# Optimization experiments

Measured on AMD Instinct MI355X. Metric: run time of the kernel, lower is better.

Reference implementation:

```python
import jax, jax.numpy as jnp
import numpy as np

B, CIN, COUT, K, SDIM, H, W = 16, 512, 512, 3, 512, 64, 64


def setup_inputs() -> dict:
    key = jax.random.key(0)
    k1, k2, k3, k4 = jax.random.split(key, 4)
    return {
        "x": jax.random.normal(k1, (B, CIN, H, W), dtype=jnp.float32),
        "style": jax.random.normal(k2, (B, SDIM), dtype=jnp.float32),
        "weight": jax.random.normal(k3, (COUT, CIN, K, K), dtype=jnp.float32),
        "style_w": jax.random.normal(k4, (CIN, SDIM), dtype=jnp.float32),
        "style_b": jnp.ones((CIN,), dtype=jnp.float32),  # bias.data.fill_(1.0)
    }


def reference(x, style, weight, style_w, style_b):
    batch, in_ch, h, w_size = x.shape
    out_ch, _, ks, _ = weight.shape
    pad = ks // 2
    # EqualizedLinear: runtime weight scaling by 1/sqrt(fan_in)
    lin_scale = 1.0 / np.sqrt(style_w.shape[1])
    s = style @ (style_w * lin_scale).T + style_b  # [B, Cin]
    # modulate
    conv_scale = 1.0 / np.sqrt(in_ch * ks * ks)
    wmod = (weight[None] * conv_scale) * s[:, None, :, None, None]  # [B,Cout,Cin,k,k]
    # demodulate
    dcoef = jax.lax.rsqrt(jnp.sum(jnp.square(wmod), axis=(2, 3, 4)) + 1e-8)  # [B,Cout]
    wmod = wmod * dcoef[:, :, None, None, None]
    # grouped conv with groups = batch
    x_r = x.reshape(1, batch * in_ch, h, w_size)
    w_r = wmod.reshape(batch * out_ch, in_ch, ks, ks)
    out = jax.lax.conv_general_dilated(
        x_r, w_r,
        window_strides=(1, 1),
        padding=[(pad, pad), (pad, pad)],
        dimension_numbers=("NCHW", "OIHW", "NCHW"),
        feature_group_count=batch,
    )
    return out.reshape(batch, out_ch, h, w_size)
```

## Files before the change

### kernel.cpp

```cpp
#include <hip/hip_runtime.h>
#include <math.h>

#define B 16
#define CIN 512
#define COUT 512
#define SDIM 512
#define H 64
#define W 64

typedef short s16x8 __attribute__((ext_vector_type(8)));
typedef float f32x4 __attribute__((ext_vector_type(4)));
typedef float f32x16 __attribute__((ext_vector_type(16)));

__device__ __constant__ float LIN_SCALE  = 0.04419417382415922f;
__device__ __constant__ float CONV_SCALE = 0.014731391274719742f;

__device__ __forceinline__ ushort f2bf(float f) {
  unsigned u = __float_as_uint(f);
  return (ushort)((u + 0x7FFFu + ((u >> 16) & 1u)) >> 16);
}

__device__ __forceinline__ int slot_swz(int col, int o) {
  return ((col & 1) * 4 + o) ^ ((col >> 1) & 7);
}

#define GLOAD16(g, l)                                           \
  __builtin_amdgcn_global_load_lds(                             \
      (const __attribute__((address_space(1))) unsigned*)(g),   \
      (__attribute__((address_space(3))) unsigned*)(l), 16, 0, 0)

__global__ __launch_bounds__(512) void style_mod_kernel(
    const float* __restrict__ style, const float* __restrict__ style_w,
    const float* __restrict__ style_b, float* __restrict__ s,
    float* __restrict__ s2) {
  const int b = blockIdx.x;
  const int ci = threadIdx.x;
  __shared__ float st[SDIM];
  st[ci] = style[b * SDIM + ci];
  __syncthreads();

  const float4* wr = reinterpret_cast<const float4*>(style_w + (size_t)ci * SDIM);
  float acc = 0.f;
#pragma unroll 4
  for (int k = 0; k < SDIM / 4; ++k) {
    float4 wv = wr[k];
    acc += st[4 * k + 0] * wv.x + st[4 * k + 1] * wv.y +
           st[4 * k + 2] * wv.z + st[4 * k + 3] * wv.w;
  }
  float v = acc * LIN_SCALE + style_b[ci];
  s[b * CIN + ci] = v;
  s2[b * CIN + ci] = v * v;
}

__global__ __launch_bounds__(512) void dcoef_kernel(
    const float* __restrict__ s2, const float* __restrict__ wsq,
    float* __restrict__ outscale) {
  const int b = blockIdx.x;
  const int co = threadIdx.x;
  __shared__ float sh[CIN];
  sh[co] = s2[b * CIN + co];
  __syncthreads();

  const float4* wr = reinterpret_cast<const float4*>(wsq + (size_t)co * CIN);
  float acc = 0.f;
#pragma unroll 4
  for (int k = 0; k < CIN / 4; ++k) {
    float4 wv = wr[k];
    acc += sh[4 * k + 0] * wv.x + sh[4 * k + 1] * wv.y +
           sh[4 * k + 2] * wv.z + sh[4 * k + 3] * wv.w;
  }
  float d = rsqrtf(acc * CONV_SCALE * CONV_SCALE + 1e-8f);
  outscale[b * COUT + co] = d * CONV_SCALE;
}

__global__ __launch_bounds__(256) void pack_w_kernel(
    const float* __restrict__ w, ushort* __restrict__ wt,
    float* __restrict__ wsq) {
  const int t = blockIdx.x * 256 + threadIdx.x;
  const int s = t & 3;
  const int chunk = (t >> 2) & 15;
  const int co = t >> 6;
  const float4* wp =
      (const float4*)(w + ((size_t)co * 512 + chunk * 32 + s * 8) * 9);
  float wv[72];
#pragma unroll
  for (int i = 0; i < 18; ++i) {
    float4 v = wp[i];
    wv[4 * i + 0] = v.x; wv[4 * i + 1] = v.y;
    wv[4 * i + 2] = v.z; wv[4 * i + 3] = v.w;
  }
  {
    float q[8];
#pragma unroll
    for (int i = 0; i < 8; ++i) {
      float a = 0.f;
#pragma unroll
      for (int k = 0; k < 9; ++k) {
        float v = wv[i * 9 + k];
        a += v * v;
      }
      q[i] = a;
    }
    float4* qd = (float4*)(wsq + (size_t)co * 512 + chunk * 32 + s * 8);
    qd[0] = make_float4(q[0], q[1], q[2], q[3]);
    qd[1] = make_float4(q[4], q[5], q[6], q[7]);
  }
  const int sp = slot_swz(co, s);
  ushort* dst = wt + (size_t)chunk * 147456 + (size_t)(co >> 1) * 64 + sp * 8;
#pragma unroll
  for (int j = 0; j < 9; ++j) {
    s16x8 p;
#pragma unroll
    for (int i = 0; i < 8; ++i) p[i] = (short)f2bf(wv[i * 9 + j]);
    *(s16x8*)(dst + (size_t)j * 16384) = p;
  }
}

__global__ __launch_bounds__(256) void pack_x_kernel(
    const float* __restrict__ x, const float* __restrict__ smod,
    ushort* __restrict__ xp) {
  __shared__ float xt[32][65];
  __shared__ float sm[32];
  const int tid = threadIdx.x;
  const int gr = blockIdx.x, chunk = blockIdx.y, b = blockIdx.z;
  if (tid < 32) sm[tid] = smod[b * 512 + chunk * 32 + tid];
  {
    const int ci = tid >> 3, cq = tid & 7;
    const float4* rp = (const float4*)(
        x + (((size_t)b * 512 + chunk * 32 + ci) * 64 + gr) * 64 + cq * 8);
    float4 a = rp[0], c2 = rp[1];
    float* row = &xt[ci][cq * 8];
    row[0] = a.x; row[1] = a.y; row[2] = a.z; row[3] = a.w;
    row[4] = c2.x; row[5] = c2.y; row[6] = c2.z; row[7] = c2.w;
  }
  __syncthreads();
  const int c = tid >> 2, o = tid & 3;
  s16x8 p;
#pragma unroll
  for (int i = 0; i < 8; ++i)
    p[i] = (short)f2bf(xt[o * 8 + i][c] * sm[o * 8 + i]);
  const int cc = c + 1;
  const int off_us = (cc >> 1) * 64 + slot_swz(cc, o) * 8 - 32;
  *(s16x8*)(xp + ((size_t)(b * 16 + chunk) * 64 + gr) * 2048 + off_us) = p;
}

#define XS4OFF 36864
#define DLDS4 79104

__global__ __launch_bounds__(256, 2) void conv_mfma6_kernel(
    const ushort* __restrict__ wt, const ushort* __restrict__ xp,
    const float* __restrict__ outscale, float* __restrict__ out) {
  extern __shared__ char smem[];

  const int tid = threadIdx.x;
  const int hb = blockIdx.x;
  const int cb = blockIdx.y;
  const int b  = blockIdx.z;
  const int h0 = hb * 8, co0 = cb * 64;
  const int lane = tid & 63, wid = tid >> 6;
  const int l31 = lane & 31, hi = lane >> 5;

  {
    s16x8* p = (s16x8*)(smem + XS4OFF);
    for (int e = tid; e < 2640; e += 256) p[e] = (s16x8)0;
  }

  f32x16 acc[2][2][2];
#pragma unroll
  for (int rr = 0; rr < 2; ++rr)
#pragma unroll
    for (int mt = 0; mt < 2; ++mt)
#pragma unroll
      for (int nt = 0; nt < 2; ++nt) acc[rr][mt][nt] = (f32x16)0.f;

  int aoff[2][2];
#pragma unroll
  for (int mt = 0; mt < 2; ++mt)
#pragma unroll
    for (int ks = 0; ks < 2; ++ks) {
      int co = mt * 32 + l31;
      aoff[mt][ks] = (co >> 1) * 128 + slot_swz(co, ks * 2 + hi) * 16;
    }
  int boff[3][2][2];
#pragma unroll
  for (int kw = 0; kw < 3; ++kw)
#pragma unroll
    for (int nt = 0; nt < 2; ++nt)
#pragma unroll
      for (int ks = 0; ks < 2; ++ks) {
        int cc = nt * 32 + l31 + kw;
        boff[kw][nt][ks] = (cc >> 1) * 128 + slot_swz(cc, ks * 2 + hi) * 16;
      }

  const char* wsrc0 = (const char*)wt + cb * 4096 + tid * 16;
  const char* xsrc0 = (const char*)xp + (size_t)b * 4194304 + tid * 16;
  char* wdst = smem + tid * 16;
  char* xdst = smem + XS4OFF + 64 + tid * 16;
  const char* wb = smem;
  const char* xb = smem + XS4OFF + 2 * wid * 4224;

  __syncthreads();

  for (int chunk = 0; chunk < 16; ++chunk) {
    const char* wsrc = wsrc0 + (size_t)chunk * 294912;
    const char* xsrc = xsrc0 + (size_t)chunk * 262144;
#pragma unroll
    for (int t = 0; t < 9; ++t)
      GLOAD16(wsrc + t * 32768, wdst + t * 4096);
#pragma unroll
    for (int t = 0; t < 10; ++t) {
      int gr = h0 - 1 + t;
      if ((unsigned)gr < 64u)
        GLOAD16(xsrc + (size_t)gr * 4096, xdst + t * 4224);
    }
    __syncthreads();

#pragma unroll
    for (int kw = 0; kw < 3; ++kw) {
      s16x8 bf[4][2][2];
#pragma unroll
      for (int q = 0; q < 4; ++q)
#pragma unroll
        for (int nt = 0; nt < 2; ++nt)
#pragma unroll
          for (int ks = 0; ks < 2; ++ks)
            bf[q][nt][ks] =
                *(const s16x8*)(xb + q * 4224 + boff[kw][nt][ks]);
#pragma unroll
      for (int kh = 0; kh < 3; ++kh) {
        const char* wj = wb + (kh * 3 + kw) * 4096;
#pragma unroll
        for (int ks = 0; ks < 2; ++ks) {
          s16x8 af0 = *(const s16x8*)(wj + aoff[0][ks]);
          s16x8 af1 = *(const s16x8*)(wj + aoff[1][ks]);
#pragma unroll
          for (int rr = 0; rr < 2; ++rr)
#pragma unroll
            for (int nt = 0; nt < 2; ++nt) {
              acc[rr][0][nt] = __builtin_amdgcn_mfma_f32_32x32x16_bf16(
                  af0, bf[rr + kh][nt][ks], acc[rr][0][nt], 0, 0, 0);
              acc[rr][1][nt] = __builtin_amdgcn_mfma_f32_32x32x16_bf16(
                  af1, bf[rr + kh][nt][ks], acc[rr][1][nt], 0, 0, 0);
            }
        }
      }
    }
    __syncthreads();
  }

#pragma unroll
  for (int mt = 0; mt < 2; ++mt) {
#pragma unroll
    for (int reg = 0; reg < 16; ++reg) {
      const int row = (reg & 3) + 8 * (reg >> 2) + 4 * hi;
      const int co = co0 + mt * 32 + row;
      const float osc = outscale[b * COUT + co];
      float* obase = out + ((size_t)b * COUT + co) * H * W;
#pragma unroll
      for (int rr = 0; rr < 2; ++rr) {
        const int h = h0 + 2 * wid + rr;
#pragma unroll
        for (int nt = 0; nt < 2; ++nt)
          obase[h * W + nt * 32 + l31] = acc[rr][mt][nt][reg] * osc;
      }
    }
  }
}

__global__ __launch_bounds__(256, 2) void conv_mfma_kernel(
    const float* __restrict__ x, const float* __restrict__ weight,
    const float* __restrict__ s, const float* __restrict__ outscale,
    float* __restrict__ out) {
  __shared__ ushort xs[6][66][32];
  __shared__ ushort ws[9][64][32];

  const int tid = threadIdx.x;
  const int hb = blockIdx.x;
  const int cb = blockIdx.y;
  const int b  = blockIdx.z;
  const int h0 = hb * 4;
  const int co0 = cb * 64;
  const int lane = tid & 63;
  const int wid = tid >> 6;
  const int l15 = lane & 15;
  const int l4  = lane >> 4;

  f32x4 acc[4][4];
#pragma unroll
  for (int mt = 0; mt < 4; ++mt)
#pragma unroll
    for (int nt = 0; nt < 4; ++nt) acc[mt][nt] = (f32x4)0.f;

  const int wq = tid & 3;
  const int wco = tid >> 2;

  for (int c0 = 0; c0 < CIN; c0 += 32) {
    {
      const float4* wp = reinterpret_cast<const float4*>(
          weight + ((size_t)(co0 + wco) * CIN + c0 + wq * 8) * 9);
      float wv[72];
#pragma unroll
      for (int t = 0; t < 18; ++t) {
        float4 v = wp[t];
        wv[4 * t + 0] = v.x; wv[4 * t + 1] = v.y;
        wv[4 * t + 2] = v.z; wv[4 * t + 3] = v.w;
      }
      float sv[8];
#pragma unroll
      for (int i = 0; i < 8; ++i) sv[i] = s[b * CIN + c0 + wq * 8 + i];
#pragma unroll
      for (int j = 0; j < 9; ++j) {
        s16x8 p;
#pragma unroll
        for (int i = 0; i < 8; ++i)
          p[i] = (short)f2bf(wv[i * 9 + j] * sv[i]);
        *reinterpret_cast<s16x8*>(&ws[j][wco][wq * 8]) = p;
      }
    }
#pragma unroll
    for (int it = 0; it < 7; ++it) {
      int e = tid + it * 256;
      if (e < 6 * 66 * 4) {
        int q = e & 3;
        int t2 = e >> 2;
        int cc = t2 % 66;
        int r = t2 / 66;
        int gr = h0 - 1 + r;
        int gc = cc - 1;
        s16x8 p;
        if ((unsigned)gr < H && (unsigned)gc < W) {
          const float* xp2 =
              x + (((size_t)b * CIN + c0 + q * 8) * H + gr) * W + gc;
#pragma unroll
          for (int i = 0; i < 8; ++i) p[i] = (short)f2bf(xp2[(size_t)i * H * W]);
        } else {
#pragma unroll
          for (int i = 0; i < 8; ++i) p[i] = 0;
        }
        *reinterpret_cast<s16x8*>(&xs[r][cc][q * 8]) = p;
      }
    }
    __syncthreads();

#pragma unroll
    for (int kh = 0; kh < 3; ++kh) {
#pragma unroll
      for (int kw = 0; kw < 3; ++kw) {
        const int j = kh * 3 + kw;
        s16x8 af[4], bf[4];
#pragma unroll
        for (int mt = 0; mt < 4; ++mt)
          af[mt] = *reinterpret_cast<const s16x8*>(
              &ws[j][mt * 16 + l15][l4 * 8]);
#pragma unroll
        for (int nt = 0; nt < 4; ++nt)
          bf[nt] = *reinterpret_cast<const s16x8*>(
              &xs[wid + kh][nt * 16 + l15 + kw][l4 * 8]);
#pragma unroll
        for (int mt = 0; mt < 4; ++mt)
#pragma unroll
          for (int nt = 0; nt < 4; ++nt)
            acc[mt][nt] = __builtin_amdgcn_mfma_f32_16x16x32_bf16(
                af[mt], bf[nt], acc[mt][nt], 0, 0, 0);
      }
    }
    __syncthreads();
  }

  const int h = h0 + wid;
#pragma unroll
  for (int mt = 0; mt < 4; ++mt) {
#pragma unroll
    for (int r = 0; r < 4; ++r) {
      const int co = co0 + mt * 16 + l4 * 4 + r;
      const float osc = outscale[b * COUT + co];
      float* orow = out + (((size_t)b * COUT + co) * H + h) * W;
#pragma unroll
      for (int nt = 0; nt < 4; ++nt)
        orow[nt * 16 + l15] = acc[mt][nt][r] * osc;
    }
  }
}

extern "C" void kernel_launch(void* const* d_in, const int* in_sizes, int n_in,
                              void* d_out, int out_size, void* d_ws,
                              size_t ws_size, hipStream_t stream) {
  const float* x = (const float*)d_in[0];
  const float* style = (const float*)d_in[1];
  const float* weight = (const float*)d_in[2];
  const float* style_w = (const float*)d_in[3];
  const float* style_b = (const float*)d_in[4];
  float* out = (float*)d_out;

  char* wsb = (char*)d_ws;
  float* s = (float*)(wsb + 0);
  float* s2 = (float*)(wsb + 32768);
  float* wsq = (float*)(wsb + 65536);
  float* outscale = (float*)(wsb + 1114112);
  ushort* wt = (ushort*)(wsb + 1146880);
  ushort* xp = (ushort*)(wsb + 5865472);
  const size_t NEED = 72974336;

  hipError_t attr_ok = hipFuncSetAttribute(
      reinterpret_cast<const void*>(conv_mfma6_kernel),
      hipFuncAttributeMaxDynamicSharedMemorySize, DLDS4);

  style_mod_kernel<<<B, 512, 0, stream>>>(style, style_w, style_b, s, s2);
  pack_w_kernel<<<128, 256, 0, stream>>>(weight, wt, wsq);
  dcoef_kernel<<<B, 512, 0, stream>>>(s2, wsq, outscale);

  if (attr_ok == hipSuccess && ws_size >= NEED) {
    pack_x_kernel<<<dim3(64, 16, 16), 256, 0, stream>>>(x, s, xp);
    conv_mfma6_kernel<<<dim3(8, 8, 16), 256, DLDS4, stream>>>(wt, xp, outscale,
                                                              out);
  } else {
    conv_mfma_kernel<<<dim3(16, 8, 16), 256, 0, stream>>>(x, weight, s,
                                                          outscale, out);
  }
}
```

Measured before the change: 345.4 us.

## Load weight MFMA fragments directly from global into registers with prefetch

Weights are repacked into per-lane MFMA fragment order so each wave reads A operands straight from global memory into registers, triple-buffered two taps ahead. This removes the weight tile from LDS, which shrinks shared memory and drops the LDS staging and reads for weights. The grid axes are also swapped so blocks sharing an input row run close together, improving reuse of the input in L2. In exchange, every wave fetches the weights itself from global or L2 memory, and the extra fragment registers raise register pressure.

```diff
diff --git a/kernel.cpp b/kernel.cpp
--- a/kernel.cpp
+++ b/kernel.cpp
@@ -105,14 +105,14 @@
     qd[0] = make_float4(q[0], q[1], q[2], q[3]);
     qd[1] = make_float4(q[4], q[5], q[6], q[7]);
   }
-  const int sp = slot_swz(co, s);
-  ushort* dst = wt + (size_t)chunk * 147456 + (size_t)(co >> 1) * 64 + sp * 8;
 #pragma unroll
   for (int j = 0; j < 9; ++j) {
     s16x8 p;
 #pragma unroll
     for (int i = 0; i < 8; ++i) p[i] = (short)f2bf(wv[i * 9 + j]);
-    *(s16x8*)(dst + (size_t)j * 16384) = p;
+    size_t frag = ((size_t)(chunk * 9 + j) * 16 + (co >> 5)) * 2 + (s >> 1);
+    size_t off = frag * 512 + (size_t)((s & 1) * 32 + (co & 31)) * 8;
+    *(s16x8*)(wt + off) = p;
   }
 }
 
@@ -144,24 +144,31 @@
   *(s16x8*)(xp + ((size_t)(b * 16 + chunk) * 64 + gr) * 2048 + off_us) = p;
 }
 
-#define XS4OFF 36864
-#define DLDS4 79104
-
-__global__ __launch_bounds__(256, 2) void conv_mfma6_kernel(
+#define DLDS7 42240
+
+#define LOADA(CK, T, BUF) {                                          \
+    const int j_ = ((T) % 3) * 3 + ((T) / 3);                        \
+    const size_t f0_ = ((size_t)((CK) * 9 + j_) * 16 + cb * 2) * 2;  \
+    af[BUF][0][0] = wfr[(f0_ + 0) * 64 + lane];                      \
+    af[BUF][0][1] = wfr[(f0_ + 1) * 64 + lane];                      \
+    af[BUF][1][0] = wfr[(f0_ + 2) * 64 + lane];                      \
+    af[BUF][1][1] = wfr[(f0_ + 3) * 64 + lane]; }
+
+__global__ __launch_bounds__(256, 2) void conv_mfma7_kernel(
     const ushort* __restrict__ wt, const ushort* __restrict__ xp,
     const float* __restrict__ outscale, float* __restrict__ out) {
   extern __shared__ char smem[];
 
   const int tid = threadIdx.x;
-  const int hb = blockIdx.x;
-  const int cb = blockIdx.y;
+  const int cb = blockIdx.x;
+  const int hb = blockIdx.y;
   const int b  = blockIdx.z;
   const int h0 = hb * 8, co0 = cb * 64;
   const int lane = tid & 63, wid = tid >> 6;
   const int l31 = lane & 31, hi = lane >> 5;
 
   {
-    s16x8* p = (s16x8*)(smem + XS4OFF);
+    s16x8* p = (s16x8*)smem;
     for (int e = tid; e < 2640; e += 256) p[e] = (s16x8)0;
   }
 
@@ -173,14 +180,6 @@
 #pragma unroll
       for (int nt = 0; nt < 2; ++nt) acc[rr][mt][nt] = (f32x16)0.f;
 
-  int aoff[2][2];
-#pragma unroll
-  for (int mt = 0; mt < 2; ++mt)
-#pragma unroll
-    for (int ks = 0; ks < 2; ++ks) {
-      int co = mt * 32 + l31;
-      aoff[mt][ks] = (co >> 1) * 128 + slot_swz(co, ks * 2 + hi) * 16;
-    }
   int boff[3][2][2];
 #pragma unroll
   for (int kw = 0; kw < 3; ++kw)
@@ -192,21 +191,19 @@
         boff[kw][nt][ks] = (cc >> 1) * 128 + slot_swz(cc, ks * 2 + hi) * 16;
       }
 
-  const char* wsrc0 = (const char*)wt + cb * 4096 + tid * 16;
   const char* xsrc0 = (const char*)xp + (size_t)b * 4194304 + tid * 16;
-  char* wdst = smem + tid * 16;
-  char* xdst = smem + XS4OFF + 64 + tid * 16;
-  const char* wb = smem;
-  const char* xb = smem + XS4OFF + 2 * wid * 4224;
+  char* xdst = smem + 64 + tid * 16;
+  const char* xb = smem + 2 * wid * 4224;
+  const s16x8* wfr = (const s16x8*)wt;
 
   __syncthreads();
 
+  s16x8 af[3][2][2];
+  LOADA(0, 0, 0);
+  LOADA(0, 1, 1);
+
   for (int chunk = 0; chunk < 16; ++chunk) {
-    const char* wsrc = wsrc0 + (size_t)chunk * 294912;
     const char* xsrc = xsrc0 + (size_t)chunk * 262144;
-#pragma unroll
-    for (int t = 0; t < 9; ++t)
-      GLOAD16(wsrc + t * 32768, wdst + t * 4096);
 #pragma unroll
     for (int t = 0; t < 10; ++t) {
       int gr = h0 - 1 + t;
@@ -215,35 +212,46 @@
     }
     __syncthreads();
 
-#pragma unroll
-    for (int kw = 0; kw < 3; ++kw) {
-      s16x8 bf[4][2][2];
-#pragma unroll
-      for (int q = 0; q < 4; ++q)
+    s16x8 bf[4][2][2];
+#pragma unroll
+    for (int t = 0; t < 9; ++t) {
+      const int kw = t / 3, kh = t % 3;
+      if (kh == 0) {
+#pragma unroll
+        for (int q = 0; q < 2; ++q)
+#pragma unroll
+          for (int nt = 0; nt < 2; ++nt)
+#pragma unroll
+            for (int ks = 0; ks < 2; ++ks)
+              bf[q][nt][ks] =
+                  *(const s16x8*)(xb + q * 4224 + boff[kw][nt][ks]);
+      }
+      if (kh < 2) {
+        const int q = kh + 2;
 #pragma unroll
         for (int nt = 0; nt < 2; ++nt)
 #pragma unroll
           for (int ks = 0; ks < 2; ++ks)
             bf[q][nt][ks] =
                 *(const s16x8*)(xb + q * 4224 + boff[kw][nt][ks]);
-#pragma unroll
-      for (int kh = 0; kh < 3; ++kh) {
-        const char* wj = wb + (kh * 3 + kw) * 4096;
-#pragma unroll
-        for (int ks = 0; ks < 2; ++ks) {
-          s16x8 af0 = *(const s16x8*)(wj + aoff[0][ks]);
-          s16x8 af1 = *(const s16x8*)(wj + aoff[1][ks]);
-#pragma unroll
-          for (int rr = 0; rr < 2; ++rr)
-#pragma unroll
-            for (int nt = 0; nt < 2; ++nt) {
-              acc[rr][0][nt] = __builtin_amdgcn_mfma_f32_32x32x16_bf16(
-                  af0, bf[rr + kh][nt][ks], acc[rr][0][nt], 0, 0, 0);
-              acc[rr][1][nt] = __builtin_amdgcn_mfma_f32_32x32x16_bf16(
-                  af1, bf[rr + kh][nt][ks], acc[rr][1][nt], 0, 0, 0);
-            }
-        }
-      }
+      }
+      if (t < 7) {
+        LOADA(chunk, t + 2, (t + 2) % 3);
+      } else {
+        LOADA((chunk + 1) & 15, t - 7, (t + 2) % 3);
+      }
+      const int cur = t % 3;
+#pragma unroll
+      for (int ks = 0; ks < 2; ++ks)
+#pragma unroll
+        for (int rr = 0; rr < 2; ++rr)
+#pragma unroll
+          for (int nt = 0; nt < 2; ++nt) {
+            acc[rr][0][nt] = __builtin_amdgcn_mfma_f32_32x32x16_bf16(
+                af[cur][0][ks], bf[rr + kh][nt][ks], acc[rr][0][nt], 0, 0, 0);
+            acc[rr][1][nt] = __builtin_amdgcn_mfma_f32_32x32x16_bf16(
+                af[cur][1][ks], bf[rr + kh][nt][ks], acc[rr][1][nt], 0, 0, 0);
+          }
     }
     __syncthreads();
   }
@@ -402,8 +410,8 @@
   const size_t NEED = 72974336;
 
   hipError_t attr_ok = hipFuncSetAttribute(
-      reinterpret_cast<const void*>(conv_mfma6_kernel),
-      hipFuncAttributeMaxDynamicSharedMemorySize, DLDS4);
+      reinterpret_cast<const void*>(conv_mfma7_kernel),
+      hipFuncAttributeMaxDynamicSharedMemorySize, DLDS7);
 
   style_mod_kernel<<<B, 512, 0, stream>>>(style, style_w, style_b, s, s2);
   pack_w_kernel<<<128, 256, 0, stream>>>(weight, wt, wsq);
@@ -411,7 +419,7 @@
 
   if (attr_ok == hipSuccess && ws_size >= NEED) {
     pack_x_kernel<<<dim3(64, 16, 16), 256, 0, stream>>>(x, s, xp);
-    conv_mfma6_kernel<<<dim3(8, 8, 16), 256, DLDS4, stream>>>(wt, xp, outscale,
+    conv_mfma7_kernel<<<dim3(8, 8, 16), 256, DLDS7, stream>>>(wt, xp, outscale,
                                                               out);
   } else {
     conv_mfma_kernel<<<dim3(16, 8, 16), 256, 0, stream>>>(x, weight, s,
```

New measurement: 367.4 us. 6.4% more time.

## Replace swizzled LDS layout with k-slot-major layout, merge prep kernels, add setprio

Applied to the files above, without the earlier changes.

Packs weights and activations in a k-slot-major layout: each 16-byte slot index owns a contiguous plane of 64 columns. The activation plane is padded to 1056 bytes, replacing the XOR swizzle and simplifying LDS address computation in the MFMA conv kernel. Fuses the style modulation and weight packing kernels into one launch to save a kernel launch, and raises wave priority around the MFMA block. The padded layout has to avoid LDS bank conflicts as well as the swizzle did, otherwise the change costs time.

```diff
diff --git a/kernel.cpp b/kernel.cpp
--- a/kernel.cpp
+++ b/kernel.cpp
@@ -20,36 +20,80 @@
   return (ushort)((u + 0x7FFFu + ((u >> 16) & 1u)) >> 16);
 }
 
-__device__ __forceinline__ int slot_swz(int col, int o) {
-  return ((col & 1) * 4 + o) ^ ((col >> 1) & 7);
-}
-
 #define GLOAD16(g, l)                                           \
   __builtin_amdgcn_global_load_lds(                             \
       (const __attribute__((address_space(1))) unsigned*)(g),   \
       (__attribute__((address_space(3))) unsigned*)(l), 16, 0, 0)
 
-__global__ __launch_bounds__(512) void style_mod_kernel(
-    const float* __restrict__ style, const float* __restrict__ style_w,
-    const float* __restrict__ style_b, float* __restrict__ s,
+__global__ __launch_bounds__(256) void prep1_kernel(
+    const float* __restrict__ w, const float* __restrict__ style,
+    const float* __restrict__ style_w, const float* __restrict__ style_b,
+    ushort* __restrict__ wt, float* __restrict__ wsq, float* __restrict__ s,
     float* __restrict__ s2) {
-  const int b = blockIdx.x;
-  const int ci = threadIdx.x;
-  __shared__ float st[SDIM];
-  st[ci] = style[b * SDIM + ci];
-  __syncthreads();
-
-  const float4* wr = reinterpret_cast<const float4*>(style_w + (size_t)ci * SDIM);
-  float acc = 0.f;
+  const int tid = threadIdx.x;
+  if (blockIdx.x < 128) {
+    const int t = blockIdx.x * 256 + tid;
+    const int so = t & 3;
+    const int chunk = (t >> 2) & 15;
+    const int co = t >> 6;
+    const float4* wp =
+        (const float4*)(w + ((size_t)co * 512 + chunk * 32 + so * 8) * 9);
+    float wv[72];
+#pragma unroll
+    for (int i = 0; i < 18; ++i) {
+      float4 v = wp[i];
+      wv[4 * i + 0] = v.x; wv[4 * i + 1] = v.y;
+      wv[4 * i + 2] = v.z; wv[4 * i + 3] = v.w;
+    }
+    {
+      float q[8];
+#pragma unroll
+      for (int i = 0; i < 8; ++i) {
+        float a = 0.f;
+#pragma unroll
+        for (int k = 0; k < 9; ++k) {
+          float v = wv[i * 9 + k];
+          a += v * v;
+        }
+        q[i] = a;
+      }
+      float4* qd = (float4*)(wsq + (size_t)co * 512 + chunk * 32 + so * 8);
+      qd[0] = make_float4(q[0], q[1], q[2], q[3]);
+      qd[1] = make_float4(q[4], q[5], q[6], q[7]);
+    }
+    const int cb = co >> 6, co64 = co & 63;
+    ushort* dst = wt + (size_t)chunk * 147456 + (size_t)cb * 2048 +
+                  (size_t)so * 512 + (size_t)co64 * 8;
+#pragma unroll
+    for (int j = 0; j < 9; ++j) {
+      s16x8 p;
+#pragma unroll
+      for (int i = 0; i < 8; ++i) p[i] = (short)f2bf(wv[i * 9 + j]);
+      *(s16x8*)(dst + (size_t)j * 16384) = p;
+    }
+  } else {
+    const int bb = blockIdx.x - 128;
+    __shared__ float st[SDIM];
+    st[tid] = style[bb * SDIM + tid];
+    st[tid + 256] = style[bb * SDIM + tid + 256];
+    __syncthreads();
+#pragma unroll
+    for (int half = 0; half < 2; ++half) {
+      const int ci = tid + half * 256;
+      const float4* wr =
+          reinterpret_cast<const float4*>(style_w + (size_t)ci * SDIM);
+      float acc = 0.f;
 #pragma unroll 4
-  for (int k = 0; k < SDIM / 4; ++k) {
-    float4 wv = wr[k];
-    acc += st[4 * k + 0] * wv.x + st[4 * k + 1] * wv.y +
-           st[4 * k + 2] * wv.z + st[4 * k + 3] * wv.w;
-  }
-  float v = acc * LIN_SCALE + style_b[ci];
-  s[b * CIN + ci] = v;
-  s2[b * CIN + ci] = v * v;
+      for (int k = 0; k < SDIM / 4; ++k) {
+        float4 wv = wr[k];
+        acc += st[4 * k + 0] * wv.x + st[4 * k + 1] * wv.y +
+               st[4 * k + 2] * wv.z + st[4 * k + 3] * wv.w;
+      }
+      float v = acc * LIN_SCALE + style_b[ci];
+      s[bb * CIN + ci] = v;
+      s2[bb * CIN + ci] = v * v;
+    }
+  }
 }
 
 __global__ __launch_bounds__(512) void dcoef_kernel(
@@ -71,49 +115,6 @@
   }
   float d = rsqrtf(acc * CONV_SCALE * CONV_SCALE + 1e-8f);
   outscale[b * COUT + co] = d * CONV_SCALE;
-}
-
-__global__ __launch_bounds__(256) void pack_w_kernel(
-    const float* __restrict__ w, ushort* __restrict__ wt,
-    float* __restrict__ wsq) {
-  const int t = blockIdx.x * 256 + threadIdx.x;
-  const int s = t & 3;
-  const int chunk = (t >> 2) & 15;
-  const int co = t >> 6;
-  const float4* wp =
-      (const float4*)(w + ((size_t)co * 512 + chunk * 32 + s * 8) * 9);
-  float wv[72];
-#pragma unroll
-  for (int i = 0; i < 18; ++i) {
-    float4 v = wp[i];
-    wv[4 * i + 0] = v.x; wv[4 * i + 1] = v.y;
-    wv[4 * i + 2] = v.z; wv[4 * i + 3] = v.w;
-  }
-  {
-    float q[8];
-#pragma unroll
-    for (int i = 0; i < 8; ++i) {
-      float a = 0.f;
-#pragma unroll
-      for (int k = 0; k < 9; ++k) {
-        float v = wv[i * 9 + k];
-        a += v * v;
-      }
-      q[i] = a;
-    }
-    float4* qd = (float4*)(wsq + (size_t)co * 512 + chunk * 32 + s * 8);
-    qd[0] = make_float4(q[0], q[1], q[2], q[3]);
-    qd[1] = make_float4(q[4], q[5], q[6], q[7]);
-  }
-  const int sp = slot_swz(co, s);
-  ushort* dst = wt + (size_t)chunk * 147456 + (size_t)(co >> 1) * 64 + sp * 8;
-#pragma unroll
-  for (int j = 0; j < 9; ++j) {
-    s16x8 p;
-#pragma unroll
-    for (int i = 0; i < 8; ++i) p[i] = (short)f2bf(wv[i * 9 + j]);
-    *(s16x8*)(dst + (size_t)j * 16384) = p;
-  }
 }
 
 __global__ __launch_bounds__(256) void pack_x_kernel(
@@ -134,20 +135,19 @@
     row[4] = c2.x; row[5] = c2.y; row[6] = c2.z; row[7] = c2.w;
   }
   __syncthreads();
-  const int c = tid >> 2, o = tid & 3;
+  const int c = tid & 63, o = tid >> 6;
   s16x8 p;
 #pragma unroll
   for (int i = 0; i < 8; ++i)
     p[i] = (short)f2bf(xt[o * 8 + i][c] * sm[o * 8 + i]);
-  const int cc = c + 1;
-  const int off_us = (cc >> 1) * 64 + slot_swz(cc, o) * 8 - 32;
-  *(s16x8*)(xp + ((size_t)(b * 16 + chunk) * 64 + gr) * 2048 + off_us) = p;
-}
-
-#define XS4OFF 36864
-#define DLDS4 79104
-
-__global__ __launch_bounds__(256, 2) void conv_mfma6_kernel(
+  *(s16x8*)(xp + ((size_t)(b * 16 + chunk) * 64 + gr) * 2048 + o * 512 +
+            c * 8) = p;
+}
+
+#define XSOFF8 36864
+#define DLDS8 79104
+
+__global__ __launch_bounds__(256, 2) void conv_mfma8_kernel(
     const ushort* __restrict__ wt, const ushort* __restrict__ xp,
     const float* __restrict__ outscale, float* __restrict__ out) {
   extern __shared__ char smem[];
@@ -161,7 +161,7 @@
   const int l31 = lane & 31, hi = lane >> 5;
 
   {
-    s16x8* p = (s16x8*)(smem + XS4OFF);
+    s16x8* p = (s16x8*)(smem + XSOFF8);
     for (int e = tid; e < 2640; e += 256) p[e] = (s16x8)0;
   }
 
@@ -177,27 +177,25 @@
 #pragma unroll
   for (int mt = 0; mt < 2; ++mt)
 #pragma unroll
-    for (int ks = 0; ks < 2; ++ks) {
-      int co = mt * 32 + l31;
-      aoff[mt][ks] = (co >> 1) * 128 + slot_swz(co, ks * 2 + hi) * 16;
-    }
+    for (int ks = 0; ks < 2; ++ks)
+      aoff[mt][ks] = (ks * 2 + hi) * 1024 + (mt * 32 + l31) * 16;
   int boff[3][2][2];
 #pragma unroll
   for (int kw = 0; kw < 3; ++kw)
 #pragma unroll
     for (int nt = 0; nt < 2; ++nt)
 #pragma unroll
-      for (int ks = 0; ks < 2; ++ks) {
-        int cc = nt * 32 + l31 + kw;
-        boff[kw][nt][ks] = (cc >> 1) * 128 + slot_swz(cc, ks * 2 + hi) * 16;
-      }
-
-  const char* wsrc0 = (const char*)wt + cb * 4096 + tid * 16;
-  const char* xsrc0 = (const char*)xp + (size_t)b * 4194304 + tid * 16;
-  char* wdst = smem + tid * 16;
-  char* xdst = smem + XS4OFF + 64 + tid * 16;
+      for (int ks = 0; ks < 2; ++ks)
+        boff[kw][nt][ks] =
+            (ks * 2 + hi) * 1056 + (nt * 32 + l31 + kw) * 16;
+
+  const char* wsrc0 = (const char*)wt + cb * 4096 + wid * 1024 + lane * 16;
+  const char* xsrc0 =
+      (const char*)xp + (size_t)b * 4194304 + wid * 1024 + lane * 16;
+  char* wdst = smem + wid * 1024 + lane * 16;
+  char* xdst = smem + XSOFF8 + wid * 1056 + 16 + lane * 16;
   const char* wb = smem;
-  const char* xb = smem + XS4OFF + 2 * wid * 4224;
+  const char* xb = smem + XSOFF8 + 2 * wid * 4224;
 
   __syncthreads();
 
@@ -233,6 +231,7 @@
         for (int ks = 0; ks < 2; ++ks) {
           s16x8 af0 = *(const s16x8*)(wj + aoff[0][ks]);
           s16x8 af1 = *(const s16x8*)(wj + aoff[1][ks]);
+          __builtin_amdgcn_s_setprio(1);
 #pragma unroll
           for (int rr = 0; rr < 2; ++rr)
 #pragma unroll
@@ -242,6 +241,7 @@
               acc[rr][1][nt] = __builtin_amdgcn_mfma_f32_32x32x16_bf16(
                   af1, bf[rr + kh][nt][ks], acc[rr][1][nt], 0, 0, 0);
             }
+          __builtin_amdgcn_s_setprio(0);
         }
       }
     }
@@ -402,18 +402,20 @@
   const size_t NEED = 72974336;
 
   hipError_t attr_ok = hipFuncSetAttribute(
-      reinterpret_cast<const void*>(conv_mfma6_kernel),
-      hipFuncAttributeMaxDynamicSharedMemorySize, DLDS4);
-
-  style_mod_kernel<<<B, 512, 0, stream>>>(style, style_w, style_b, s, s2);
-  pack_w_kernel<<<128, 256, 0, stream>>>(weight, wt, wsq);
-  dcoef_kernel<<<B, 512, 0, stream>>>(s2, wsq, outscale);
+      reinterpret_cast<const void*>(conv_mfma8_kernel),
+      hipFuncAttributeMaxDynamicSharedMemorySize, DLDS8);
 
   if (attr_ok == hipSuccess && ws_size >= NEED) {
+    prep1_kernel<<<144, 256, 0, stream>>>(weight, style, style_w, style_b, wt,
+                                          wsq, s, s2);
+    dcoef_kernel<<<B, 512, 0, stream>>>(s2, wsq, outscale);
     pack_x_kernel<<<dim3(64, 16, 16), 256, 0, stream>>>(x, s, xp);
-    conv_mfma6_kernel<<<dim3(8, 8, 16), 256, DLDS4, stream>>>(wt, xp, outscale,
+    conv_mfma8_kernel<<<dim3(8, 8, 16), 256, DLDS8, stream>>>(wt, xp, outscale,
                                                               out);
   } else {
+    prep1_kernel<<<144, 256, 0, stream>>>(weight, style, style_w, style_b, wt,
+                                          wsq, s, s2);
+    dcoef_kernel<<<B, 512, 0, stream>>>(s2, wsq, outscale);
     conv_mfma_kernel<<<dim3(16, 8, 16), 256, 0, stream>>>(x, weight, s,
                                                           outscale, out);
   }
```

Measured after the change: 352.4 us. 1.02x slower.
